# Kernel tuning notes

Measured on AMD Instinct MI355X. Metric: run time of the kernel, lower is better.

The kernel has to match this reference:

```python
import jax, jax.numpy as jnp
import numpy as np

N, E, B, D, H = 5000, 16000, 8, 128, 8
HD = D // H
DD = D // 2  # diachronic dim (gamma = 0.5)
V, R = 20000, 500


def setup_inputs() -> dict:
    key = jax.random.key(0)
    ks = jax.random.split(key, 28)
    f = lambda i, shape, s=0.05: (jax.random.normal(ks[i], shape, jnp.float32) * s)
    inp = {
        "src": jax.random.randint(ks[0], (E,), 0, N),
        "dst": jax.random.randint(ks[1], (E,), 0, N),
        "node_idx": jax.random.randint(ks[2], (N,), 0, V),
        "relation_type": jax.random.randint(ks[3], (E,), 1, R),
        "edge_start": jax.random.randint(ks[4], (E,), 0, 365),
        "edge_end": jax.random.randint(ks[5], (E,), 0, 365),
        "batch_start": jax.random.randint(ks[6], (B,), 0, 365),
        "batch_end": jax.random.randint(ks[7], (B,), 0, 365),
        "node_time": jax.random.uniform(ks[8], (N,), jnp.float32, 0.0, 365.0),
        "edge_t2v": f(9, (E, D), 1.0),
        "batch_t2v": f(10, (B, D), 1.0),
        "syn_embed": f(11, (V, D)),
        "dia_embed": f(12, (V, DD)),
        "dia_w": f(13, (V, DD)),
        "dia_b": f(14, (V, DD)),
        "rel_embed": f(15, (R, D)),
        "ts_W1": f(16, (2 * D, 4 * D)),
        "ts_b1": jnp.zeros((4 * D,), jnp.float32),
        "ts_W2": f(17, (4 * D, 2 * D)),
        "ts_b2": jnp.zeros((2 * D,), jnp.float32),
        "ts_W3": f(18, (2 * D, D)),
        "ts_b3": jnp.zeros((D,), jnp.float32),
        "W_ss": f(19, (3, D, D)),
        "b_ss": jnp.zeros((3, D), jnp.float32),
        "W_ee": f(20, (3, D, D)),
        "b_ee": jnp.zeros((3, D), jnp.float32),
        "attn_i": f(21, (H, HD), 0.1),
        "attn_j": f(22, (H, HD), 0.1),
    }
    return inp


def _lin3(x, idx, W, b):
    # x: (E,B,D); idx: (E,B) in {0:past,1:present,2:future}; W: (3,D,D); b: (3,D)
    out = jnp.zeros_like(x)
    for k in range(3):
        out = out + jnp.where((idx == k)[..., None], x @ W[k] + b[k], 0.0)
    return out


def reference(src, dst, node_idx, relation_type, edge_start, edge_end,
              batch_start, batch_end, node_time, edge_t2v, batch_t2v,
              syn_embed, dia_embed, dia_w, dia_b, rel_embed,
              ts_W1, ts_b1, ts_W2, ts_b2, ts_W3, ts_b3,
              W_ss, b_ss, W_ee, b_ee, attn_i, attn_j):
    # diachronic node embedding: synchronic + sin-modulated diachronic half
    h_n = syn_embed[node_idx]                                   # (N, D)
    dia = dia_embed[node_idx] * jnp.sin(
        dia_w[node_idx] * node_time[:, None] + dia_b[node_idx])  # (N, DD)
    h_n = h_n.at[:, DD:].add(dia)

    # tau: per-(edge, query) time score via MLP 2D -> 4D -> 2D -> D
    x = jnp.concatenate([
        jnp.broadcast_to(edge_t2v[:, None, :], (E, B, D)),
        jnp.broadcast_to(batch_t2v[None, :, :], (E, B, D))], axis=-1)
    h = jax.nn.relu(x @ ts_W1 + ts_b1)
    h = jax.nn.relu(h @ ts_W2 + ts_b2)
    tau = h @ ts_W3 + ts_b3                                      # (E, B, D)

    # time-type (past/present/future) selector per edge per query
    idx_ss = (jnp.sign(edge_start[:, None] - batch_start[None, :]) + 1).astype(jnp.int32)
    idx_ee = (jnp.sign(edge_end[:, None] - batch_end[None, :]) + 1).astype(jnp.int32)

    h_e = rel_embed[relation_type]                               # (E, D)
    g_e = (_lin3(h_n[src][:, None, :] + tau, idx_ss, W_ss, b_ss)
           + _lin3(h_e[:, None, :] + tau, idx_ee, W_ee, b_ee))   # (E, B, D)
    g_e = g_e.reshape(E, B, H, HD)

    # GAT-style scores: (dst-node * attn_i) * (edge * attn_j), elementwise per head
    ai = h_n.reshape(N, 1, H, HD) * attn_i                       # (N, 1, H, HD)
    score = jax.nn.leaky_relu(ai[dst] * (g_e * attn_j))          # (E, B, H, HD)

    # edge softmax per destination node (segment softmax over dst)
    m = jax.ops.segment_max(score, dst, num_segments=N)
    s = jnp.exp(score - m[dst])
    z = jax.ops.segment_sum(s, dst, num_segments=N)
    a = s / (z[dst] + 1e-16)

    h_new = jax.ops.segment_sum(a * g_e, dst, num_segments=N)    # (N, B, H, HD)
    return jax.nn.leaky_relu(h_new.reshape(N, B, D))
```

## Files before the change

### kernel.cpp

```cpp
#include <hip/hip_runtime.h>
#include <hip/hip_bf16.h>

typedef __attribute__((ext_vector_type(8))) short short8;
typedef __attribute__((ext_vector_type(4))) float f32x4;

#define N_NODES 5000
#define E_EDGES 16000
#define B_Q 8
#define D_DIM 128

#define OFF_U     0
#define OFF_G     4096000
#define OFF_HN    12288000
#define OFF_WDST  12928000
#define OFF_VB    13568000
#define OFF_W1T   13572096
#define OFF_W2T   13604864
#define OFF_W3T   13670400
#define OFF_WALLT 13686784
#define OFF_CNT   13735936
#define OFF_ROWP  13740936
#define OFF_CUR   13745937
#define OFF_ECSR  13750937

__device__ __forceinline__ float leaky(float x) { return x > 0.f ? x : 0.01f * x; }
__device__ __forceinline__ int sgnk(int a, int b) { int d = a - b; return d > 0 ? 2 : (d == 0 ? 1 : 0); }
__device__ __forceinline__ unsigned short f2bf(float f) {
    __hip_bfloat16 h = __float2bfloat16(f);
    unsigned short r; __builtin_memcpy(&r, &h, 2); return r;
}
__device__ __forceinline__ unsigned pk2(float a, float b) {
    return (unsigned)f2bf(a) | ((unsigned)f2bf(b) << 16);
}
__device__ __forceinline__ float bflo(unsigned w) { return __uint_as_float(w << 16); }
__device__ __forceinline__ float bfhi(unsigned w) { return __uint_as_float(w & 0xffff0000u); }
__device__ __forceinline__ float bf2f(unsigned short s) { return __uint_as_float(((unsigned)s) << 16); }

#define SWZB(row, lb)  (((row) << 7) + ((lb) ^ (((row) & 7) << 4)))
#define SWZ256(row, lb) (((row) << 8) + ((lb) ^ (((row) & 7) << 4)))
#define SWZ512(row, lb) (((row) << 9) + ((lb) ^ (((row) & 7) << 4)))

__global__ void k_wprep(const float* __restrict__ W1, const float* __restrict__ W2,
                        const float* __restrict__ W3, const float* __restrict__ Wss,
                        const float* __restrict__ Wee,
                        ushort* __restrict__ W1t, ushort* __restrict__ W2t,
                        ushort* __restrict__ W3t, ushort* __restrict__ Wallt) {
    int tid = blockIdx.x * 256 + threadIdx.x;
    if (tid < 131072) {
        int n = tid >> 9, k = tid & 511;
        W2t[tid] = f2bf(W2[k * 256 + n]);
    } else if (tid < 163840) {
        int q = tid - 131072; int n = q >> 8, k = q & 255;
        W3t[q] = f2bf(W3[k * 128 + n]);
    } else if (tid < 262144) {
        int q = tid - 163840; int c = q >> 14, rr = q & 16383, n = rr >> 7, k = rr & 127;
        const float* Wm = (c < 3) ? Wss : Wee; int cc = (c < 3) ? c : c - 3;
        Wallt[q] = f2bf(Wm[cc * 16384 + k * 128 + n]);
    } else if (tid < 327680) {
        int q = tid - 262144; int n = q >> 7, k = q & 127;
        W1t[q] = f2bf(W1[k * 512 + n]);
    }
}

__global__ void k_node(const int* __restrict__ node_idx, const float* __restrict__ node_time,
                       const float* __restrict__ syn, const float* __restrict__ diae,
                       const float* __restrict__ diaw, const float* __restrict__ diab,
                       const float* __restrict__ attn_i, const float* __restrict__ attn_j,
                       float* __restrict__ h_n, float* __restrict__ w_dst) {
    int n = blockIdx.x, d = threadIdx.x;
    int nid = node_idx[n];
    float h = syn[nid * D_DIM + d];
    if (d >= 64) {
        int q = d - 64;
        h += diae[nid * 64 + q] * sinf(diaw[nid * 64 + q] * node_time[n] + diab[nid * 64 + q]);
    }
    h_n[n * D_DIM + d] = h;
    w_dst[n * D_DIM + d] = h * attn_i[d] * attn_j[d];
}

__global__ void k_vb(const float* __restrict__ bt2v, const float* __restrict__ W1,
                     const float* __restrict__ b1, float* __restrict__ v_b) {
    int b = blockIdx.x, j = threadIdx.x;
    float acc = b1[j];
    for (int i = 0; i < 128; ++i)
        acc = fmaf(bt2v[b * 128 + i], W1[(128 + i) * 512 + j], acc);
    v_b[b * 512 + j] = acc;
}

__global__ void k_count(const int* __restrict__ dst, int* __restrict__ cnt) {
    int e = blockIdx.x * 256 + threadIdx.x;
    if (e < E_EDGES) atomicAdd(&cnt[dst[e]], 1);
}

__global__ void k_scan(const int* __restrict__ cnt, int* __restrict__ rowptr,
                       int* __restrict__ cursor) {
    __shared__ int part[256];
    const int t = threadIdx.x;
    const int i0 = t * 20, i1 = min(N_NODES, i0 + 20);
    int s = 0;
    for (int i = i0; i < i1; ++i) s += cnt[i];
    part[t] = s;
    __syncthreads();
    for (int off = 1; off < 256; off <<= 1) {
        int v = (t >= off) ? part[t - off] : 0;
        __syncthreads();
        part[t] += v;
        __syncthreads();
    }
    int run = (t > 0) ? part[t - 1] : 0;
    for (int i = i0; i < i1; ++i) { rowptr[i] = run; cursor[i] = run; run += cnt[i]; }
    if (i0 < N_NODES && i1 == N_NODES) rowptr[N_NODES] = run;
}

__global__ void k_scatter(const int* __restrict__ dst, int* __restrict__ cursor,
                          int* __restrict__ ecsr) {
    int e = blockIdx.x * 256 + threadIdx.x;
    if (e < E_EDGES) {
        int p = atomicAdd(&cursor[dst[e]], 1);
        ecsr[p] = e;
    }
}

__device__ __forceinline__ void mfma_step(const unsigned char* lA, const unsigned char* lB,
                                          int wr, int wc, int lane, f32x4 (&acc)[4][4]) {
    const int row0 = wr * 64 + (lane & 15);
    const int nrow0 = wc * 64 + (lane & 15);
    const int kslot = (lane >> 4) * 16;
#pragma unroll
    for (int ks = 0; ks < 2; ++ks) {
        short8 a[4], b[4];
#pragma unroll
        for (int m = 0; m < 4; ++m)
            a[m] = *(const short8*)(lA + SWZB(row0 + m * 16, ks * 64 + kslot));
#pragma unroll
        for (int n = 0; n < 4; ++n)
            b[n] = *(const short8*)(lB + SWZB(nrow0 + n * 16, ks * 64 + kslot));
#pragma unroll
        for (int m = 0; m < 4; ++m)
#pragma unroll
            for (int n = 0; n < 4; ++n)
                acc[m][n] = __builtin_amdgcn_mfma_f32_16x16x32_bf16(a[m], b[n], acc[m][n], 0, 0, 0);
    }
}

__global__ __launch_bounds__(256) void k_gemm1(const float* __restrict__ et2v,
                                               const ushort* __restrict__ W1t,
                                               ushort* __restrict__ u) {
    __shared__ __align__(16) unsigned char lA[16384];
    __shared__ __align__(16) unsigned char lB[16384];
    const int t = threadIdx.x;
    const int m0 = (blockIdx.x >> 2) * 128;
    const int n0 = (blockIdx.x & 3) * 128;
    const int lane = t & 63, wid = t >> 6, wr = wid >> 1, wc = wid & 1;
    const int srow = t >> 1, koff = (t & 1) * 32, lb0 = (t & 1) * 64;
    f32x4 acc[4][4] = {};
    for (int step = 0; step < 2; ++step) {
        const float4* ap = (const float4*)(et2v + (size_t)(m0 + srow) * 128 + step * 64 + koff);
#pragma unroll
        for (int i = 0; i < 4; ++i) {
            float4 x0 = ap[2 * i], x1 = ap[2 * i + 1];
            *(uint4*)&lA[SWZB(srow, lb0 + i * 16)] =
                make_uint4(pk2(x0.x, x0.y), pk2(x0.z, x0.w), pk2(x1.x, x1.y), pk2(x1.z, x1.w));
        }
        const uint4* bp = (const uint4*)(W1t + (size_t)(n0 + srow) * 128 + step * 64 + koff);
#pragma unroll
        for (int i = 0; i < 4; ++i) *(uint4*)&lB[SWZB(srow, lb0 + i * 16)] = bp[i];
        __syncthreads();
        mfma_step(lA, lB, wr, wc, lane, acc);
        __syncthreads();
    }
    const int rbase = wr * 64 + ((lane >> 4) << 2);
    const int cbase = n0 + wc * 64 + (lane & 15);
#pragma unroll
    for (int mm = 0; mm < 4; ++mm)
#pragma unroll
        for (int nn = 0; nn < 4; ++nn)
#pragma unroll
            for (int i = 0; i < 4; ++i)
                u[(size_t)(m0 + rbase + mm * 16 + i) * 512 + cbase + nn * 16] =
                    f2bf(acc[mm][nn][i]);
}

__global__ __launch_bounds__(256, 2) void k_mega(
    const ushort* __restrict__ u, const float* __restrict__ v_b,
    const ushort* __restrict__ W2t, const float* __restrict__ b2,
    const ushort* __restrict__ W3t, const float* __restrict__ b3,
    const ushort* __restrict__ Wallt,
    const float* __restrict__ bss, const float* __restrict__ bee,
    const int* __restrict__ src, const int* __restrict__ rtyp,
    const int* __restrict__ edge_start, const int* __restrict__ edge_end,
    const int* __restrict__ batch_start, const int* __restrict__ batch_end,
    const float* __restrict__ h_n, const float* __restrict__ rel_embed,
    ushort* __restrict__ g_e) {
    __shared__ __align__(16) unsigned char lds[65536];
    __shared__ int selss_s[128], selee_s[128];
    __shared__ int am_s;
    const int t = threadIdx.x;
    const int m0 = blockIdx.x * 128;
    const int lane = t & 63, wid = t >> 6, wr = wid >> 1, wc = wid & 1;
    const int srow = t >> 1, koff = (t & 1) * 32, lb0 = (t & 1) * 64;
    const int l15 = lane & 15;
    const int ls4 = (lane >> 4) << 2;
    const int kslot = (lane >> 4) * 16;
    const int kslot8 = (lane >> 4) * 8;

    if (t == 0) am_s = 0;
    __syncthreads();
    if (t < 128) {
        const int gr = m0 + t, e = gr >> 3, b = gr & 7;
        const int ss = sgnk(edge_start[e], batch_start[b]);
        const int se = sgnk(edge_end[e], batch_end[b]);
        selss_s[t] = ss; selee_s[t] = se;
        atomicOr(&am_s, (1 << ss) | (8 << se));
    }

    unsigned char* lA = lds;
    unsigned char* lB = lds + 16384;
    const int ae = (m0 + srow) >> 3, ab = (m0 + srow) & 7;
    f32x4 acc2[4][8] = {};
    for (int step = 0; step < 8; ++step) {
        const int k0 = step * 64;
        const uint4* up = (const uint4*)(u + (size_t)ae * 512 + k0 + koff);
        const float4* vp = (const float4*)(v_b + ab * 512 + k0 + koff);
#pragma unroll
        for (int i = 0; i < 4; ++i) {
            uint4 uv = up[i];
            float4 va = vp[2 * i], vb4 = vp[2 * i + 1];
            unsigned r0 = pk2(fmaxf(bflo(uv.x) + va.x, 0.f), fmaxf(bfhi(uv.x) + va.y, 0.f));
            unsigned r1 = pk2(fmaxf(bflo(uv.y) + va.z, 0.f), fmaxf(bfhi(uv.y) + va.w, 0.f));
            unsigned r2 = pk2(fmaxf(bflo(uv.z) + vb4.x, 0.f), fmaxf(bfhi(uv.z) + vb4.y, 0.f));
            unsigned r3 = pk2(fmaxf(bflo(uv.w) + vb4.z, 0.f), fmaxf(bfhi(uv.w) + vb4.w, 0.f));
            *(uint4*)&lA[SWZB(srow, lb0 + i * 16)] = make_uint4(r0, r1, r2, r3);
        }
        const uint4* bp = (const uint4*)(W2t + (size_t)t * 512 + k0);
#pragma unroll
        for (int i = 0; i < 8; ++i) *(uint4*)&lB[SWZB(t, i * 16)] = bp[i];
        __syncthreads();
        {
            const int row0 = wr * 64 + l15;
            const int nrow0 = wc * 128 + l15;
#pragma unroll
            for (int ks = 0; ks < 2; ++ks) {
                short8 a[4], b[8];
#pragma unroll
                for (int m = 0; m < 4; ++m)
                    a[m] = *(const short8*)(lA + SWZB(row0 + m * 16, ks * 64 + kslot));
#pragma unroll
                for (int n = 0; n < 8; ++n)
                    b[n] = *(const short8*)(lB + SWZB(nrow0 + n * 16, ks * 64 + kslot));
#pragma unroll
                for (int m = 0; m < 4; ++m)
#pragma unroll
                    for (int n = 0; n < 8; ++n)
                        acc2[m][n] = __builtin_amdgcn_mfma_f32_16x16x32_bf16(a[m], b[n], acc2[m][n], 0, 0, 0);
            }
        }
        __syncthreads();
    }

    const int rb = wr * 64 + ls4;
    const int cb2 = wc * 128 + l15;
    float b2r[8];
#pragma unroll
    for (int nn = 0; nn < 8; ++nn) b2r[nn] = b2[cb2 + nn * 16];
#pragma unroll
    for (int mm = 0; mm < 4; ++mm)
#pragma unroll
        for (int i = 0; i < 4; ++i) {
            const int r = rb + mm * 16 + i;
#pragma unroll
            for (int nn = 0; nn < 8; ++nn) {
                const int k = cb2 + nn * 16;
                *(ushort*)&lds[SWZ512(r, 2 * k)] =
                    f2bf(fmaxf(acc2[mm][nn][i] + b2r[nn], 0.f));
            }
        }
    __syncthreads();

    f32x4 tacc[4][4] = {};
#pragma unroll
    for (int ks = 0; ks < 8; ++ks) {
        short8 a[4], b[4];
#pragma unroll
        for (int m = 0; m < 4; ++m) {
            const int rA = wr * 64 + l15 + m * 16;
            a[m] = *(const short8*)&lds[SWZ512(rA, ks * 64 + kslot)];
        }
#pragma unroll
        for (int n = 0; n < 4; ++n) {
            const int nB = wc * 64 + l15 + n * 16;
            b[n] = *(const short8*)(W3t + nB * 256 + ks * 32 + kslot8);
        }
#pragma unroll
        for (int m = 0; m < 4; ++m)
#pragma unroll
            for (int n = 0; n < 4; ++n)
                tacc[m][n] = __builtin_amdgcn_mfma_f32_16x16x32_bf16(a[m], b[n], tacc[m][n], 0, 0, 0);
    }
    __syncthreads();

    const int cb1 = wc * 64 + l15;
    float b3r[4];
#pragma unroll
    for (int nn = 0; nn < 4; ++nn) b3r[nn] = b3[cb1 + nn * 16];
#pragma unroll
    for (int mm = 0; mm < 4; ++mm)
#pragma unroll
        for (int i = 0; i < 4; ++i) {
            const int r = rb + mm * 16 + i;
            const int gr = m0 + r, e = gr >> 3;
            const int se = src[e], rr = rtyp[e];
#pragma unroll
            for (int nn = 0; nn < 4; ++nn) {
                const int k2 = cb1 + nn * 16;
                const float tau = tacc[mm][nn][i] + b3r[nn];
                *(ushort*)&lds[SWZ256(r, 2 * k2)] = f2bf(h_n[se * 128 + k2] + tau);
                *(ushort*)&lds[32768 + SWZ256(r, 2 * k2)] = f2bf(rel_embed[rr * 128 + k2] + tau);
            }
        }
    __syncthreads();

    int sel_ss[4], sel_ee[4];
#pragma unroll
    for (int m = 0; m < 4; ++m) {
        const int rA = wr * 64 + l15 + m * 16;
        sel_ss[m] = selss_s[rA]; sel_ee[m] = selee_s[rA];
    }
    const int am = am_s;
    const short8 zero8 = {0, 0, 0, 0, 0, 0, 0, 0};
    f32x4 gacc[4][4] = {};
    for (int c = 0; c < 6; ++c) {
        if (!((am >> c) & 1)) continue;
        const int m3 = (c < 3) ? c : c - 3;
        const int xb = (c < 3) ? 0 : 32768;
#pragma unroll
        for (int ks = 0; ks < 4; ++ks) {
            short8 a[4], b[4];
#pragma unroll
            for (int m = 0; m < 4; ++m) {
                const int rA = wr * 64 + l15 + m * 16;
                short8 v = *(const short8*)&lds[xb + SWZ256(rA, ks * 64 + kslot)];
                const int sel = (c < 3) ? sel_ss[m] : sel_ee[m];
                a[m] = (sel == m3) ? v : zero8;
            }
#pragma unroll
            for (int n = 0; n < 4; ++n) {
                const int nB = wc * 64 + l15 + n * 16;
                b[n] = *(const short8*)(Wallt + (size_t)c * 16384 + nB * 128 + ks * 32 + kslot8);
            }
#pragma unroll
            for (int m = 0; m < 4; ++m)
#pragma unroll
                for (int n = 0; n < 4; ++n)
                    gacc[m][n] = __builtin_amdgcn_mfma_f32_16x16x32_bf16(a[m], b[n], gacc[m][n], 0, 0, 0);
        }
    }
    __syncthreads();

#pragma unroll
    for (int mm = 0; mm < 4; ++mm)
#pragma unroll
        for (int i = 0; i < 4; ++i) {
            const int r = rb + mm * 16 + i;
            const int ss = selss_s[r], se = selee_s[r];
#pragma unroll
            for (int nn = 0; nn < 4; ++nn) {
                const int k2 = cb1 + nn * 16;
                const float g = gacc[mm][nn][i] + bss[ss * 128 + k2] + bee[se * 128 + k2];
                *(ushort*)&lds[SWZ256(r, 2 * k2)] = f2bf(g);
            }
        }
    __syncthreads();
    {
        const int r = srow, half = t & 1;
        const size_t gbase = (size_t)(m0 + r) * 128 + half * 64;
#pragma unroll
        for (int q = 0; q < 8; ++q) {
            uint4 v = *(const uint4*)&lds[SWZ256(r, half * 128 + q * 16)];
            *(uint4*)(g_e + gbase + q * 8) = v;
        }
    }
}

__global__ __launch_bounds__(128) void k_segsm(const int* __restrict__ rowptr,
                                               const int* __restrict__ ecsr,
                                               const float* __restrict__ wdst,
                                               const ushort* __restrict__ g_e,
                                               float* __restrict__ out) {
    const int n = blockIdx.x, d = threadIdx.x;
    const float w = wdst[n * 128 + d];
    const int s0 = rowptr[n], s1 = rowptr[n + 1];
    float m[8], z[8], S[8];
#pragma unroll
    for (int b = 0; b < 8; ++b) { m[b] = -1e30f; z[b] = 0.f; S[b] = 0.f; }
    for (int i = s0; i < s1; ++i) {
        const int e = ecsr[i];
        const ushort* gp = g_e + (size_t)e * 1024 + d;
#pragma unroll
        for (int b = 0; b < 8; ++b) {
            float g = bf2f(gp[b * 128]);
            float sc = leaky(w * g);
            float nm = fmaxf(m[b], sc);
            float sca = __expf(m[b] - nm);
            float s = __expf(sc - nm);
            z[b] = z[b] * sca + s;
            S[b] = S[b] * sca + s * g;
            m[b] = nm;
        }
    }
#pragma unroll
    for (int b = 0; b < 8; ++b) {
        float r = S[b] / (z[b] + 1e-16f);
        out[((size_t)n * 8 + b) * 128 + d] = leaky(r);
    }
}

extern "C" void kernel_launch(void* const* d_in, const int* in_sizes, int n_in,
                              void* d_out, int out_size, void* d_ws, size_t ws_size,
                              hipStream_t stream) {
    const int* src = (const int*)d_in[0];
    const int* dst = (const int*)d_in[1];
    const int* node_idx = (const int*)d_in[2];
    const int* rel = (const int*)d_in[3];
    const int* es = (const int*)d_in[4];
    const int* eend = (const int*)d_in[5];
    const int* bs = (const int*)d_in[6];
    const int* be = (const int*)d_in[7];
    const float* node_time = (const float*)d_in[8];
    const float* edge_t2v = (const float*)d_in[9];
    const float* batch_t2v = (const float*)d_in[10];
    const float* syn = (const float*)d_in[11];
    const float* diae = (const float*)d_in[12];
    const float* diaw = (const float*)d_in[13];
    const float* diab = (const float*)d_in[14];
    const float* rele = (const float*)d_in[15];
    const float* W1 = (const float*)d_in[16];
    const float* b1 = (const float*)d_in[17];
    const float* W2 = (const float*)d_in[18];
    const float* b2 = (const float*)d_in[19];
    const float* W3 = (const float*)d_in[20];
    const float* b3 = (const float*)d_in[21];
    const float* Wss = (const float*)d_in[22];
    const float* bss = (const float*)d_in[23];
    const float* Wee = (const float*)d_in[24];
    const float* bee = (const float*)d_in[25];
    const float* ai = (const float*)d_in[26];
    const float* aj = (const float*)d_in[27];

    float* ws = (float*)d_ws;
    ushort* u = (ushort*)(ws + OFF_U);
    ushort* g_e = (ushort*)(ws + OFF_G);
    float* h_n = ws + OFF_HN;
    float* wdst = ws + OFF_WDST;
    float* v_b = ws + OFF_VB;
    ushort* W1t = (ushort*)(ws + OFF_W1T);
    ushort* W2t = (ushort*)(ws + OFF_W2T);
    ushort* W3t = (ushort*)(ws + OFF_W3T);
    ushort* Wallt = (ushort*)(ws + OFF_WALLT);
    int* cnt = (int*)(ws + OFF_CNT);
    int* rowptr = (int*)(ws + OFF_ROWP);
    int* cursor = (int*)(ws + OFF_CUR);
    int* ecsr = (int*)(ws + OFF_ECSR);
    float* out = (float*)d_out;

    hipMemsetAsync(cnt, 0, N_NODES * sizeof(int), stream);
    k_count<<<63, 256, 0, stream>>>(dst, cnt);
    k_scan<<<1, 256, 0, stream>>>(cnt, rowptr, cursor);
    k_scatter<<<63, 256, 0, stream>>>(dst, cursor, ecsr);

    k_wprep<<<1280, 256, 0, stream>>>(W1, W2, W3, Wss, Wee, W1t, W2t, W3t, Wallt);
    k_node<<<N_NODES, 128, 0, stream>>>(node_idx, node_time, syn, diae, diaw, diab, ai, aj, h_n, wdst);
    k_vb<<<B_Q, 512, 0, stream>>>(batch_t2v, W1, b1, v_b);
    k_gemm1<<<500, 256, 0, stream>>>(edge_t2v, W1t, u);
    k_mega<<<1000, 256, 0, stream>>>(u, v_b, W2t, b2, W3t, b3, Wallt, bss, bee,
                                     src, rel, es, eend, bs, be, h_n, rele, g_e);
    k_segsm<<<N_NODES, 128, 0, stream>>>(rowptr, ecsr, wdst, g_e, out);
}
```

Baseline: 339.0 us.

## Pre-gather edge features, stage GEMM1 stores via LDS, prefetch u in mega kernel

Adds a kernel that gathers h_n[src] and rel_embed[rtyp] into contiguous bf16 per-edge arrays, so the mega kernel reads them with vectorized 16-byte loads instead of scattered scalar gathers. GEMM1 output goes through LDS and is written as coalesced uint4 stores. The mega kernel register-prefetches the next u slice, and the bias epilogue uses a precomputed 9-combo bias table in LDS, adding it during the vectorized store. The cost is an extra launch and about 8 MB of extra traffic, plus an extra bf16 rounding of h_n+tau.

```diff
diff --git a/kernel.cpp b/kernel.cpp
--- a/kernel.cpp
+++ b/kernel.cpp
@@ -22,6 +22,8 @@
 #define OFF_ROWP  13740936
 #define OFF_CUR   13745937
 #define OFF_ECSR  13750937
+#define OFF_HSRC  13766944
+#define OFF_HREL  14790944
 
 __device__ __forceinline__ float leaky(float x) { return x > 0.f ? x : 0.01f * x; }
 __device__ __forceinline__ int sgnk(int a, int b) { int d = a - b; return d > 0 ? 2 : (d == 0 ? 1 : 0); }
@@ -35,6 +37,9 @@
 __device__ __forceinline__ float bflo(unsigned w) { return __uint_as_float(w << 16); }
 __device__ __forceinline__ float bfhi(unsigned w) { return __uint_as_float(w & 0xffff0000u); }
 __device__ __forceinline__ float bf2f(unsigned short s) { return __uint_as_float(((unsigned)s) << 16); }
+__device__ __forceinline__ unsigned addpk(unsigned a, unsigned b) {
+    return pk2(bflo(a) + bflo(b), bfhi(a) + bfhi(b));
+}
 
 #define SWZB(row, lb)  (((row) << 7) + ((lb) ^ (((row) & 7) << 4)))
 #define SWZ256(row, lb) (((row) << 8) + ((lb) ^ (((row) & 7) << 4)))
@@ -87,6 +92,15 @@
     v_b[b * 512 + j] = acc;
 }
 
+__global__ void k_egather(const int* __restrict__ src, const int* __restrict__ rtyp,
+                          const float* __restrict__ h_n, const float* __restrict__ rel_embed,
+                          ushort* __restrict__ hsrc, ushort* __restrict__ hrel) {
+    int idx = blockIdx.x * 256 + threadIdx.x;
+    int e = idx >> 7, d = idx & 127;
+    hsrc[idx] = f2bf(h_n[src[e] * 128 + d]);
+    hrel[idx] = f2bf(rel_embed[rtyp[e] * 128 + d]);
+}
+
 __global__ void k_count(const int* __restrict__ dst, int* __restrict__ cnt) {
     int e = blockIdx.x * 256 + threadIdx.x;
     if (e < E_EDGES) atomicAdd(&cnt[dst[e]], 1);
@@ -146,8 +160,9 @@
 __global__ __launch_bounds__(256) void k_gemm1(const float* __restrict__ et2v,
                                                const ushort* __restrict__ W1t,
                                                ushort* __restrict__ u) {
-    __shared__ __align__(16) unsigned char lA[16384];
-    __shared__ __align__(16) unsigned char lB[16384];
+    __shared__ __align__(16) unsigned char lds2[32768];
+    unsigned char* lA = lds2;
+    unsigned char* lB = lds2 + 16384;
     const int t = threadIdx.x;
     const int m0 = (blockIdx.x >> 2) * 128;
     const int n0 = (blockIdx.x & 3) * 128;
@@ -170,15 +185,24 @@
         __syncthreads();
     }
     const int rbase = wr * 64 + ((lane >> 4) << 2);
-    const int cbase = n0 + wc * 64 + (lane & 15);
+    const int cb = wc * 64 + (lane & 15);
 #pragma unroll
     for (int mm = 0; mm < 4; ++mm)
 #pragma unroll
-        for (int nn = 0; nn < 4; ++nn)
-#pragma unroll
-            for (int i = 0; i < 4; ++i)
-                u[(size_t)(m0 + rbase + mm * 16 + i) * 512 + cbase + nn * 16] =
-                    f2bf(acc[mm][nn][i]);
+        for (int i = 0; i < 4; ++i) {
+            const int r = rbase + mm * 16 + i;
+#pragma unroll
+            for (int nn = 0; nn < 4; ++nn)
+                *(ushort*)&lds2[SWZ256(r, 2 * (cb + nn * 16))] = f2bf(acc[mm][nn][i]);
+        }
+    __syncthreads();
+    {
+        const int r = t >> 1, kh = t & 1;
+        ushort* up = u + (size_t)(m0 + r) * 512 + n0 + kh * 64;
+#pragma unroll
+        for (int q = 0; q < 8; ++q)
+            *(uint4*)(up + q * 8) = *(const uint4*)&lds2[SWZ256(r, kh * 128 + q * 16)];
+    }
 }
 
 __global__ __launch_bounds__(256, 2) void k_mega(
@@ -187,22 +211,20 @@
     const ushort* __restrict__ W3t, const float* __restrict__ b3,
     const ushort* __restrict__ Wallt,
     const float* __restrict__ bss, const float* __restrict__ bee,
-    const int* __restrict__ src, const int* __restrict__ rtyp,
+    const ushort* __restrict__ hsrc, const ushort* __restrict__ hrel,
     const int* __restrict__ edge_start, const int* __restrict__ edge_end,
     const int* __restrict__ batch_start, const int* __restrict__ batch_end,
-    const float* __restrict__ h_n, const float* __restrict__ rel_embed,
     ushort* __restrict__ g_e) {
     __shared__ __align__(16) unsigned char lds[65536];
+    __shared__ __align__(16) float bsum[1152];
     __shared__ int selss_s[128], selee_s[128];
     __shared__ int am_s;
     const int t = threadIdx.x;
     const int m0 = blockIdx.x * 128;
     const int lane = t & 63, wid = t >> 6, wr = wid >> 1, wc = wid & 1;
     const int srow = t >> 1, koff = (t & 1) * 32, lb0 = (t & 1) * 64;
-    const int l15 = lane & 15;
-    const int ls4 = (lane >> 4) << 2;
-    const int kslot = (lane >> 4) * 16;
-    const int kslot8 = (lane >> 4) * 8;
+    const int l15 = lane & 15, ls4 = (lane >> 4) << 2;
+    const int kslot = (lane >> 4) * 16, kslot8 = (lane >> 4) * 8;
 
     if (t == 0) am_s = 0;
     __syncthreads();
@@ -213,18 +235,27 @@
         selss_s[t] = ss; selee_s[t] = se;
         atomicOr(&am_s, (1 << ss) | (8 << se));
     }
+    for (int idx = t; idx < 1152; idx += 256) {
+        const int combo = idx >> 7, k = idx & 127;
+        bsum[idx] = bss[(combo / 3) * 128 + k] + bee[(combo % 3) * 128 + k];
+    }
 
     unsigned char* lA = lds;
     unsigned char* lB = lds + 16384;
     const int ae = (m0 + srow) >> 3, ab = (m0 + srow) & 7;
     f32x4 acc2[4][8] = {};
+    uint4 ucur[4], unxt[4];
+    {
+        const ushort* ub = u + (size_t)ae * 512 + koff;
+#pragma unroll
+        for (int i = 0; i < 4; ++i) ucur[i] = *(const uint4*)(ub + i * 8);
+    }
     for (int step = 0; step < 8; ++step) {
         const int k0 = step * 64;
-        const uint4* up = (const uint4*)(u + (size_t)ae * 512 + k0 + koff);
         const float4* vp = (const float4*)(v_b + ab * 512 + k0 + koff);
 #pragma unroll
         for (int i = 0; i < 4; ++i) {
-            uint4 uv = up[i];
+            uint4 uv = ucur[i];
             float4 va = vp[2 * i], vb4 = vp[2 * i + 1];
             unsigned r0 = pk2(fmaxf(bflo(uv.x) + va.x, 0.f), fmaxf(bfhi(uv.x) + va.y, 0.f));
             unsigned r1 = pk2(fmaxf(bflo(uv.y) + va.z, 0.f), fmaxf(bfhi(uv.y) + va.w, 0.f));
@@ -235,6 +266,11 @@
         const uint4* bp = (const uint4*)(W2t + (size_t)t * 512 + k0);
 #pragma unroll
         for (int i = 0; i < 8; ++i) *(uint4*)&lB[SWZB(t, i * 16)] = bp[i];
+        if (step < 7) {
+            const ushort* ub = u + (size_t)ae * 512 + (k0 + 64) + koff;
+#pragma unroll
+            for (int i = 0; i < 4; ++i) unxt[i] = *(const uint4*)(ub + i * 8);
+        }
         __syncthreads();
         {
             const int row0 = wr * 64 + l15;
@@ -256,6 +292,8 @@
             }
         }
         __syncthreads();
+#pragma unroll
+        for (int i = 0; i < 4; ++i) ucur[i] = unxt[i];
     }
 
     const int rb = wr * 64 + ls4;
@@ -308,16 +346,33 @@
 #pragma unroll
         for (int i = 0; i < 4; ++i) {
             const int r = rb + mm * 16 + i;
-            const int gr = m0 + r, e = gr >> 3;
-            const int se = src[e], rr = rtyp[e];
 #pragma unroll
             for (int nn = 0; nn < 4; ++nn) {
                 const int k2 = cb1 + nn * 16;
-                const float tau = tacc[mm][nn][i] + b3r[nn];
-                *(ushort*)&lds[SWZ256(r, 2 * k2)] = f2bf(h_n[se * 128 + k2] + tau);
-                *(ushort*)&lds[32768 + SWZ256(r, 2 * k2)] = f2bf(rel_embed[rr * 128 + k2] + tau);
+                *(ushort*)&lds[SWZ256(r, 2 * k2)] = f2bf(tacc[mm][nn][i] + b3r[nn]);
             }
         }
+    __syncthreads();
+
+    {
+        const int r = t >> 1, kh = t & 1, el = r >> 3;
+        const ushort* hs = hsrc + ((size_t)(m0 >> 3) + el) * 128 + kh * 64;
+        const ushort* hr = hrel + ((size_t)(m0 >> 3) + el) * 128 + kh * 64;
+#pragma unroll
+        for (int q = 0; q < 8; ++q) {
+            const int boff = SWZ256(r, kh * 128 + q * 16);
+            uint4 tv = *(const uint4*)&lds[boff];
+            uint4 sv = *(const uint4*)(hs + q * 8);
+            uint4 rv = *(const uint4*)(hr + q * 8);
+            uint4 xs, xe;
+            xs.x = addpk(tv.x, sv.x); xs.y = addpk(tv.y, sv.y);
+            xs.z = addpk(tv.z, sv.z); xs.w = addpk(tv.w, sv.w);
+            xe.x = addpk(tv.x, rv.x); xe.y = addpk(tv.y, rv.y);
+            xe.z = addpk(tv.z, rv.z); xe.w = addpk(tv.w, rv.w);
+            *(uint4*)&lds[boff] = xs;
+            *(uint4*)&lds[32768 + boff] = xe;
+        }
+    }
     __syncthreads();
 
     int sel_ss[4], sel_ee[4];
@@ -362,22 +417,29 @@
 #pragma unroll
         for (int i = 0; i < 4; ++i) {
             const int r = rb + mm * 16 + i;
-            const int ss = selss_s[r], se = selee_s[r];
 #pragma unroll
             for (int nn = 0; nn < 4; ++nn) {
                 const int k2 = cb1 + nn * 16;
-                const float g = gacc[mm][nn][i] + bss[ss * 128 + k2] + bee[se * 128 + k2];
-                *(ushort*)&lds[SWZ256(r, 2 * k2)] = f2bf(g);
+                *(ushort*)&lds[SWZ256(r, 2 * k2)] = f2bf(gacc[mm][nn][i]);
             }
         }
     __syncthreads();
     {
-        const int r = srow, half = t & 1;
-        const size_t gbase = (size_t)(m0 + r) * 128 + half * 64;
+        const int r = t >> 1, kh = t & 1;
+        const int c9 = selss_s[r] * 3 + selee_s[r];
+        const float* bp = &bsum[c9 * 128 + kh * 64];
+        ushort* gp = g_e + (size_t)(m0 + r) * 128 + kh * 64;
 #pragma unroll
         for (int q = 0; q < 8; ++q) {
-            uint4 v = *(const uint4*)&lds[SWZ256(r, half * 128 + q * 16)];
-            *(uint4*)(g_e + gbase + q * 8) = v;
+            uint4 gv = *(const uint4*)&lds[SWZ256(r, kh * 128 + q * 16)];
+            float4 f0 = *(const float4*)(bp + q * 8);
+            float4 f1 = *(const float4*)(bp + q * 8 + 4);
+            uint4 o;
+            o.x = pk2(bflo(gv.x) + f0.x, bfhi(gv.x) + f0.y);
+            o.y = pk2(bflo(gv.y) + f0.z, bfhi(gv.y) + f0.w);
+            o.z = pk2(bflo(gv.z) + f1.x, bfhi(gv.z) + f1.y);
+            o.w = pk2(bflo(gv.w) + f1.z, bfhi(gv.w) + f1.w);
+            *(uint4*)(gp + q * 8) = o;
         }
     }
 }
@@ -461,6 +523,8 @@
     int* rowptr = (int*)(ws + OFF_ROWP);
     int* cursor = (int*)(ws + OFF_CUR);
     int* ecsr = (int*)(ws + OFF_ECSR);
+    ushort* hsrc = (ushort*)(ws + OFF_HSRC);
+    ushort* hrel = (ushort*)(ws + OFF_HREL);
     float* out = (float*)d_out;
 
     hipMemsetAsync(cnt, 0, N_NODES * sizeof(int), stream);
@@ -471,8 +535,9 @@
     k_wprep<<<1280, 256, 0, stream>>>(W1, W2, W3, Wss, Wee, W1t, W2t, W3t, Wallt);
     k_node<<<N_NODES, 128, 0, stream>>>(node_idx, node_time, syn, diae, diaw, diab, ai, aj, h_n, wdst);
     k_vb<<<B_Q, 512, 0, stream>>>(batch_t2v, W1, b1, v_b);
+    k_egather<<<E_EDGES * D_DIM / 256, 256, 0, stream>>>(src, rel, h_n, rele, hsrc, hrel);
     k_gemm1<<<500, 256, 0, stream>>>(edge_t2v, W1t, u);
     k_mega<<<1000, 256, 0, stream>>>(u, v_b, W2t, b2, W3t, b3, Wallt, bss, bee,
-                                     src, rel, es, eend, bs, be, h_n, rele, g_e);
+                                     hsrc, hrel, es, eend, bs, be, g_e);
     k_segsm<<<N_NODES, 128, 0, stream>>>(rowptr, ecsr, wdst, g_e, out);
 }
```

Result: no change. 340.3 us (+0.4%).
